# Optimization experiments

Hardware: AMD Instinct MI355X
Metric: run time of the kernel (lower is better)

Reference implementation:

```python
import jax, jax.numpy as jnp
import numpy as np

B, N, DIN, DOUT = 64, 1024, 64, 64


def setup_inputs() -> dict:
    key = jax.random.key(0)
    k1, k2, k3 = jax.random.split(key, 3)
    # adj entries in (0,1): positive row-sums so rsqrt(degree) is finite
    adj_batch = jax.random.uniform(k1, (B, N, N), dtype=jnp.float32)
    att_batch = jax.random.normal(k2, (B, N, DIN), dtype=jnp.float32)
    # xavier_uniform_ init for weight
    bound = float(np.sqrt(6.0 / (DIN + DOUT)))
    weight = jax.random.uniform(k3, (DIN, DOUT), dtype=jnp.float32,
                                minval=-bound, maxval=bound)
    return {"adj_batch": adj_batch, "att_batch": att_batch, "weight": weight}


def reference(adj_batch, att_batch, weight):
    # Degrees computed on adj BEFORE self-loops (faithful to the torch code).
    deg = jnp.sum(adj_batch, axis=-1)              # [B, N]
    dinv = jax.lax.rsqrt(deg)                      # 1/sqrt(deg), diag of D
    # s_adj = adj + I  (self-loops added AFTER degree computation)
    s_adj = adj_batch + jnp.eye(N, dtype=adj_batch.dtype)[None]  # [B, N, N]
    # out = D @ s_adj @ D @ (att @ W); diagonal matmuls fused as row scalings
    x = jnp.einsum('bnd,de->bne', att_batch, weight)   # att @ W   [B, N, DOUT]
    x = dinv[..., None] * x                             # D @ x
    y = jnp.einsum('bij,bjd->bid', s_adj, x)            # s_adj @ (D x)
    out = dinv[..., None] * y                           # D @ (...)
    return (out, weight)
```

## Files before the change

kernel.cpp:

```cpp
#include <hip/hip_runtime.h>
#include <stdint.h>
#include <stddef.h>

#define BATCH 64
#define NN    1024
#define DD    64

typedef _Float16 h8 __attribute__((ext_vector_type(8)));
typedef _Float16 h4 __attribute__((ext_vector_type(4)));
typedef float    f32x4 __attribute__((ext_vector_type(4)));

__device__ __forceinline__ int swz(int row, int gran) {
    return (row << 3) + (gran ^ (row & 7));
}

__global__ __launch_bounds__(256) void k_wt(const float* __restrict__ w,
                                            _Float16* __restrict__ wt,
                                            float* __restrict__ ow) {
#pragma unroll
    for (int it = 0; it < 4; ++it) {
        const int idx = threadIdx.x + (it << 8);
        const int k = idx >> 4, d4 = idx & 15;
        const float4 v = ((const float4*)w)[idx];
        wt[(d4 * 4 + 0) * DD + k] = (_Float16)v.x;
        wt[(d4 * 4 + 1) * DD + k] = (_Float16)v.y;
        wt[(d4 * 4 + 2) * DD + k] = (_Float16)v.z;
        wt[(d4 * 4 + 3) * DD + k] = (_Float16)v.w;
        ((float4*)ow)[idx] = v;
    }
}

__global__ __launch_bounds__(256) void k_xw(const float* __restrict__ att,
                                            const _Float16* __restrict__ wt,
                                            _Float16* __restrict__ zT) {
    __shared__ __align__(16) _Float16 attS[128 * 64];
    __shared__ __align__(16) _Float16 wtS[64 * 64];
    const int t = threadIdx.x;
    const int bb = blockIdx.y;
    const int j0 = blockIdx.x * 128;

#pragma unroll
    for (int it = 0; it < 4; ++it) {
        const int g = t + (it << 8);
        const int r = g >> 3, c = g & 7;
        const float4* p = (const float4*)(att + (size_t)(bb * NN + j0 + r) * DD + (c << 3));
        const float4 v0 = p[0], v1 = p[1];
        h8 o;
        o[0] = (_Float16)v0.x; o[1] = (_Float16)v0.y; o[2] = (_Float16)v0.z; o[3] = (_Float16)v0.w;
        o[4] = (_Float16)v1.x; o[5] = (_Float16)v1.y; o[6] = (_Float16)v1.z; o[7] = (_Float16)v1.w;
        *(h8*)&attS[swz(r, c) * 8] = o;
    }
#pragma unroll
    for (int it = 0; it < 2; ++it) {
        const int g = t + (it << 8);
        const int r = g >> 3, c = g & 7;
        const h8 v = *(const h8*)(wt + r * DD + (c << 3));
        *(h8*)&wtS[swz(r, c) * 8] = v;
    }
    __syncthreads();

    const int w = t >> 6, lane = t & 63;
    const int lr = lane & 15, lg = lane >> 4;
    const f32x4 zero = {0.f, 0.f, 0.f, 0.f};
    f32x4 acc[2][4];
#pragma unroll
    for (int mf = 0; mf < 2; ++mf)
#pragma unroll
        for (int nf = 0; nf < 4; ++nf) acc[mf][nf] = zero;

#pragma unroll
    for (int kk = 0; kk < 2; ++kk) {
        h8 a[2], bfr[4];
#pragma unroll
        for (int mf = 0; mf < 2; ++mf)
            a[mf] = *(const h8*)&attS[swz(w * 32 + mf * 16 + lr, kk * 4 + lg) * 8];
#pragma unroll
        for (int nf = 0; nf < 4; ++nf)
            bfr[nf] = *(const h8*)&wtS[swz(nf * 16 + lr, kk * 4 + lg) * 8];
#pragma unroll
        for (int mf = 0; mf < 2; ++mf)
#pragma unroll
            for (int nf = 0; nf < 4; ++nf)
                acc[mf][nf] = __builtin_amdgcn_mfma_f32_16x16x32_f16(a[mf], bfr[nf], acc[mf][nf], 0, 0, 0);
    }

#pragma unroll
    for (int mf = 0; mf < 2; ++mf) {
        const int jb = j0 + w * 32 + mf * 16 + lg * 4;
#pragma unroll
        for (int nf = 0; nf < 4; ++nf) {
            const int d = nf * 16 + lr;
            h4 o;
            o[0] = (_Float16)acc[mf][nf][0];
            o[1] = (_Float16)acc[mf][nf][1];
            o[2] = (_Float16)acc[mf][nf][2];
            o[3] = (_Float16)acc[mf][nf][3];
            *(h4*)(zT + (size_t)(bb * DD + d) * NN + jb) = o;
        }
    }
}

__global__ __launch_bounds__(256) void k_deg(const float* __restrict__ adj,
                                             float* __restrict__ dinv) {
    const int lane = threadIdx.x & 63;
    const int rowg = blockIdx.x * 4 + (threadIdx.x >> 6);
    const float* rp = adj + (size_t)rowg * NN;
    float s = 0.f;
#pragma unroll
    for (int k = 0; k < 4; ++k) {
        const float4 v = ((const float4*)rp)[lane + (k << 6)];
        s += v.x + v.y + v.z + v.w;
    }
#pragma unroll
    for (int off = 32; off; off >>= 1) s += __shfl_xor(s, off);
    if (lane == 0) dinv[rowg] = 1.f / sqrtf(s);
}

__global__ __launch_bounds__(256) void k_agg(const float* __restrict__ adj,
                                             const _Float16* __restrict__ zT,
                                             const float* __restrict__ dinv,
                                             float* __restrict__ out) {
    __shared__ __align__(16) _Float16 adjS[64 * 64];
    __shared__ __align__(16) _Float16 zS[64 * 64];
    const int t = threadIdx.x;
    const int rev = (BATCH * (NN / 64) - 1) - (blockIdx.y * gridDim.x + blockIdx.x);
    const int bb = rev >> 4;
    const int i0 = (rev & 15) << 6;
    const int w = t >> 6, lane = t & 63;
    const int lr = lane & 15, lg = lane >> 4;
    const float* dvB = dinv + bb * NN;
    const int ktDiag = i0 >> 6;

    const int r0 = t >> 3, c0 = t & 7;
    const int r1 = (t + 256) >> 3, c1 = t & 7;

    float4 pa[2][2];
    float4 pd[2][2];
    h8     pz[2];

    auto loadT = [&](int kt) {
        const int gj0 = kt * 64 + (c0 << 3);
        const float4* p0 = (const float4*)(adj + (size_t)(bb * NN + i0 + r0) * NN + gj0);
        pa[0][0] = p0[0]; pa[0][1] = p0[1];
        pd[0][0] = *(const float4*)(dvB + gj0);
        pd[0][1] = *(const float4*)(dvB + gj0 + 4);
        pz[0] = *(const h8*)(zT + (size_t)(bb * DD + r0) * NN + gj0);
        const int gj1 = kt * 64 + (c1 << 3);
        const float4* p1 = (const float4*)(adj + (size_t)(bb * NN + i0 + r1) * NN + gj1);
        pa[1][0] = p1[0]; pa[1][1] = p1[1];
        pd[1][0] = *(const float4*)(dvB + gj1);
        pd[1][1] = *(const float4*)(dvB + gj1 + 4);
        pz[1] = *(const h8*)(zT + (size_t)(bb * DD + r1) * NN + gj1);
    };
    auto writeT = [&]() {
#pragma unroll
        for (int it = 0; it < 2; ++it) {
            const int r = it ? r1 : r0, c = it ? c1 : c0;
            h8 o;
            o[0] = (_Float16)(pa[it][0].x * pd[it][0].x);
            o[1] = (_Float16)(pa[it][0].y * pd[it][0].y);
            o[2] = (_Float16)(pa[it][0].z * pd[it][0].z);
            o[3] = (_Float16)(pa[it][0].w * pd[it][0].w);
            o[4] = (_Float16)(pa[it][1].x * pd[it][1].x);
            o[5] = (_Float16)(pa[it][1].y * pd[it][1].y);
            o[6] = (_Float16)(pa[it][1].z * pd[it][1].z);
            o[7] = (_Float16)(pa[it][1].w * pd[it][1].w);
            *(h8*)&adjS[swz(r, c) * 8] = o;
            *(h8*)&zS[swz(r, c) * 8] = pz[it];
        }
    };

    const f32x4 zero = {0.f, 0.f, 0.f, 0.f};
    f32x4 acc[4];
#pragma unroll
    for (int nf = 0; nf < 4; ++nf) acc[nf] = zero;

    loadT(15);
    for (int kt = 15; kt >= 0; --kt) {
        writeT();
        if (kt == ktDiag) {
            __syncthreads();
            if (t < 64)
                adjS[swz(t, t >> 3) * 8 + (t & 7)] += (_Float16)dvB[i0 + t];
        }
        __syncthreads();
        if (kt > 0) loadT(kt - 1);
#pragma unroll
        for (int kk = 0; kk < 2; ++kk) {
            const h8 a = *(const h8*)&adjS[swz(w * 16 + lr, kk * 4 + lg) * 8];
#pragma unroll
            for (int nf = 0; nf < 4; ++nf) {
                const h8 bz = *(const h8*)&zS[swz(nf * 16 + lr, kk * 4 + lg) * 8];
                acc[nf] = __builtin_amdgcn_mfma_f32_16x16x32_f16(a, bz, acc[nf], 0, 0, 0);
            }
        }
        __syncthreads();
    }

    const int ib = i0 + w * 16 + lg * 4;
    const float4 dv = *(const float4*)&dinv[bb * NN + ib];
#pragma unroll
    for (int nf = 0; nf < 4; ++nf) {
        const int d = nf * 16 + lr;
        float* op = out + (size_t)(bb * NN + ib) * DD + d;
        __builtin_nontemporal_store(acc[nf][0] * dv.x, op + 0 * DD);
        __builtin_nontemporal_store(acc[nf][1] * dv.y, op + 1 * DD);
        __builtin_nontemporal_store(acc[nf][2] * dv.z, op + 2 * DD);
        __builtin_nontemporal_store(acc[nf][3] * dv.w, op + 3 * DD);
    }
}

extern "C" void kernel_launch(void* const* d_in, const int* in_sizes, int n_in,
                              void* d_out, int out_size, void* d_ws, size_t ws_size,
                              hipStream_t stream) {
    const float* adj = (const float*)d_in[0];
    const float* att = (const float*)d_in[1];
    const float* wgt = (const float*)d_in[2];
    float* out = (float*)d_out;
    char* ws = (char*)d_ws;

    size_t off = 0;
    _Float16* zT  = (_Float16*)(ws + off); off += (size_t)BATCH * DD * NN * 2;
    float*    dinv = (float*)(ws + off);   off += (size_t)BATCH * NN * 4;
    _Float16* wt  = (_Float16*)(ws + off);

    k_wt<<<1, 256, 0, stream>>>(wgt, wt, out + (size_t)BATCH * NN * DD);
    k_xw<<<dim3(NN / 128, BATCH), 256, 0, stream>>>(att, wt, zT);
    k_deg<<<BATCH * NN / 4, 256, 0, stream>>>(adj, dinv);
    k_agg<<<dim3(NN / 64, BATCH), 256, 0, stream>>>(adj, zT, dinv, out);
}
```

Baseline: 108.0 us.

## Fuse degree computation into aggregation kernel with per-batch atomic barrier

After: 216.7 us. +100.6%, slower.

```diff
diff --git a/kernel.cpp b/kernel.cpp
--- a/kernel.cpp
+++ b/kernel.cpp
@@ -5,6 +5,7 @@
 #define BATCH 64
 #define NN    1024
 #define DD    64
+#define CTRS  32
 
 typedef _Float16 h8 __attribute__((ext_vector_type(8)));
 typedef _Float16 h4 __attribute__((ext_vector_type(4)));
@@ -16,7 +17,10 @@
 
 __global__ __launch_bounds__(256) void k_wt(const float* __restrict__ w,
                                             _Float16* __restrict__ wt,
-                                            float* __restrict__ ow) {
+                                            float* __restrict__ ow,
+                                            int* __restrict__ ctr) {
+#pragma unroll
+    for (int z = 0; z < 8; ++z) ctr[threadIdx.x + (z << 8)] = 0;
 #pragma unroll
     for (int it = 0; it < 4; ++it) {
         const int idx = threadIdx.x + (it << 8);
@@ -100,33 +104,47 @@
     }
 }
 
-__global__ __launch_bounds__(256) void k_deg(const float* __restrict__ adj,
-                                             float* __restrict__ dinv) {
-    const int lane = threadIdx.x & 63;
-    const int rowg = blockIdx.x * 4 + (threadIdx.x >> 6);
-    const float* rp = adj + (size_t)rowg * NN;
-    float s = 0.f;
-#pragma unroll
-    for (int k = 0; k < 4; ++k) {
-        const float4 v = ((const float4*)rp)[lane + (k << 6)];
-        s += v.x + v.y + v.z + v.w;
-    }
-#pragma unroll
-    for (int off = 32; off; off >>= 1) s += __shfl_xor(s, off);
-    if (lane == 0) dinv[rowg] = 1.f / sqrtf(s);
-}
-
-__global__ __launch_bounds__(256) void k_agg(const float* __restrict__ adj,
-                                             const _Float16* __restrict__ zT,
-                                             const float* __restrict__ dinv,
-                                             float* __restrict__ out) {
+__global__ __launch_bounds__(256, 4) void k_degagg(const float* __restrict__ adj,
+                                                   const _Float16* __restrict__ zT,
+                                                   float* __restrict__ dinv,
+                                                   float* __restrict__ out,
+                                                   int* __restrict__ ctr) {
     __shared__ __align__(16) _Float16 adjS[64 * 64];
     __shared__ __align__(16) _Float16 zS[64 * 64];
     const int t = threadIdx.x;
-    const int rev = (BATCH * (NN / 64) - 1) - (blockIdx.y * gridDim.x + blockIdx.x);
-    const int bb = rev >> 4;
-    const int i0 = (rev & 15) << 6;
+    const int x = blockIdx.x;
+    const int bb = x & 63;
+    const int i0 = (x >> 6) << 6;
     const int w = t >> 6, lane = t & 63;
+
+#pragma unroll 1
+    for (int rr = 0; rr < 16; ++rr) {
+        const int gi = i0 + (w << 4) + rr;
+        const float* rp = adj + ((size_t)bb * NN + gi) * NN;
+        float s = 0.f;
+#pragma unroll
+        for (int k = 0; k < 4; ++k) {
+            const float4 v = ((const float4*)rp)[lane + (k << 6)];
+            s += v.x + v.y + v.z + v.w;
+        }
+#pragma unroll
+        for (int off = 32; off; off >>= 1) s += __shfl_xor(s, off);
+        if (lane == 0)
+            __hip_atomic_store(dinv + bb * NN + gi, 1.f / sqrtf(s),
+                               __ATOMIC_RELAXED, __HIP_MEMORY_SCOPE_AGENT);
+    }
+    __syncthreads();
+    if (t == 0)
+        __hip_atomic_fetch_add(ctr + bb * CTRS, 1, __ATOMIC_RELEASE, __HIP_MEMORY_SCOPE_AGENT);
+
+    if (t == 0) {
+        while (__hip_atomic_load(ctr + bb * CTRS, __ATOMIC_RELAXED,
+                                 __HIP_MEMORY_SCOPE_AGENT) < 16)
+            __builtin_amdgcn_s_sleep(8);
+    }
+    __syncthreads();
+    __threadfence();
+
     const int lr = lane & 15, lg = lane >> 4;
     const float* dvB = dinv + bb * NN;
     const int ktDiag = i0 >> 6;
@@ -175,8 +193,9 @@
 #pragma unroll
     for (int nf = 0; nf < 4; ++nf) acc[nf] = zero;
 
-    loadT(15);
-    for (int kt = 15; kt >= 0; --kt) {
+    loadT(0);
+#pragma unroll 1
+    for (int kt = 0; kt < 16; ++kt) {
         writeT();
         if (kt == ktDiag) {
             __syncthreads();
@@ -184,7 +203,7 @@
                 adjS[swz(t, t >> 3) * 8 + (t & 7)] += (_Float16)dvB[i0 + t];
         }
         __syncthreads();
-        if (kt > 0) loadT(kt - 1);
+        if (kt < 15) loadT(kt + 1);
 #pragma unroll
         for (int kk = 0; kk < 2; ++kk) {
             const h8 a = *(const h8*)&adjS[swz(w * 16 + lr, kk * 4 + lg) * 8];
@@ -198,11 +217,11 @@
     }
 
     const int ib = i0 + w * 16 + lg * 4;
-    const float4 dv = *(const float4*)&dinv[bb * NN + ib];
+    const float4 dv = *(const float4*)&dvB[ib];
 #pragma unroll
     for (int nf = 0; nf < 4; ++nf) {
         const int d = nf * 16 + lr;
-        float* op = out + (size_t)(bb * NN + ib) * DD + d;
+        float* op = out + ((size_t)bb * NN + ib) * DD + d;
         __builtin_nontemporal_store(acc[nf][0] * dv.x, op + 0 * DD);
         __builtin_nontemporal_store(acc[nf][1] * dv.y, op + 1 * DD);
         __builtin_nontemporal_store(acc[nf][2] * dv.z, op + 2 * DD);
@@ -222,10 +241,10 @@
     size_t off = 0;
     _Float16* zT  = (_Float16*)(ws + off); off += (size_t)BATCH * DD * NN * 2;
     float*    dinv = (float*)(ws + off);   off += (size_t)BATCH * NN * 4;
-    _Float16* wt  = (_Float16*)(ws + off);
-
-    k_wt<<<1, 256, 0, stream>>>(wgt, wt, out + (size_t)BATCH * NN * DD);
+    _Float16* wt  = (_Float16*)(ws + off); off += (size_t)DD * DD * 2;
+    int*      ctr = (int*)(ws + off);
+
+    k_wt<<<1, 256, 0, stream>>>(wgt, wt, out + (size_t)BATCH * NN * DD, ctr);
     k_xw<<<dim3(NN / 128, BATCH), 256, 0, stream>>>(att, wt, zT);
-    k_deg<<<BATCH * NN / 4, 256, 0, stream>>>(adj, dinv);
-    k_agg<<<dim3(NN / 64, BATCH), 256, 0, stream>>>(adj, zT, dinv, out);
-}
+    k_degagg<<<BATCH * (NN / 64), 256, 0, stream>>>(adj, zT, dinv, out, ctr);
+}
```
